# Kernel tuning notes

Measured on AMD Instinct MI355X. Metric: run time of the kernel, lower is better.

Reference implementation:

```python
import jax, jax.numpy as jnp
import numpy as np

PI = 3.1415927410125732
N = 4096
VELOCITY = 5e-7
RC = 3.15e-6          # collision radius
RR = 8e-6             # repulsion radius
RO = 2.5e-5           # orientation radius (Ra = inf -> inside_Ra all-true)
ALPHA = PI            # field of view; < 2*pi so within_view masking is active
DT_TRANS = 1.4e-14    # translational diffusion DT
DR = 0.0028
GAMMA = 25.0
DT = 0.2              # timestep dt
COLLISION_ITERS = 3   # fixed-iteration version of recursive solve_collisions
EPS = 1e-14


def _c(x):  # [N,2] real -> complex64
    return jax.lax.complex(x[..., 0], x[..., 1])


def _r(z):  # complex -> [..., 2] real
    return jnp.stack([z.real, z.imag], axis=-1)


def _anglediff(a, b):
    # torch get_anglediff: wrap angle(a)-angle(b) into (-pi, pi)
    diff = jnp.angle(a) - jnp.angle(b)
    diff = jnp.where(diff <= -PI, jnp.mod(diff, PI), diff)
    return diff - (diff >= PI) * (2.0 * PI)


def _cossim(a, b):
    # nn.CosineSimilarity(dim=1, eps=1e-14) on view_as_real of complex vectors
    dot = a.real * b.real + a.imag * b.imag
    na = jnp.sqrt(a.real ** 2 + a.imag ** 2 + 1e-30)
    nb = jnp.sqrt(b.real ** 2 + b.imag ** 2 + 1e-30)
    return dot / (jnp.maximum(na, EPS) * jnp.maximum(nb, EPS))


def setup_inputs() -> dict:
    key = jax.random.key(0)
    k1, k2, k3, k4, k5 = jax.random.split(key, 5)
    positions = jax.random.normal(k1, (N, 2), jnp.float32) * 5e-4
    ang = jax.random.uniform(k2, (N,), jnp.float32, -PI, PI)
    orientations = jnp.stack([jnp.cos(ang), jnp.sin(ang)], axis=-1)  # unit complex
    Deltas = jax.random.uniform(k3, (1,), jnp.float32, 0.1, 0.6)
    rot_noise = jax.random.normal(k4, (N,), jnp.float32)
    trans_noise = jax.random.normal(k5, (N, 2), jnp.float32)
    return {"positions": positions, "orientations": orientations, "Deltas": Deltas,
            "rot_noise": rot_noise, "trans_noise": trans_noise}


def reference(positions, orientations, Deltas, rot_noise, trans_noise):
    p = _c(positions)      # [N] complex positions
    u = _c(orientations)   # [N] complex orientations
    n = p.shape[0]
    eye = jnp.eye(n, dtype=bool)

    # pairwise direction/distance: dirs[i,j] = p_j - p_i
    dirs = p[None, :] - p[:, None]
    dists = jnp.abs(dirs)

    inside_Rr = (dists <= RR) & ~eye
    inside_Ro = dists <= RO + RC
    # inside_Ra with Ra = inf is all-True

    # angle between separation vector and orientation of the *neighbor* j
    ang_diff = _anglediff(dirs, u[None, :])
    in_front = ang_diff < PI / 2
    within_view = ang_diff < ALPHA  # alpha < 2*pi branch active

    cdtype = p.dtype
    mask_rr = (inside_Rr & in_front).astype(cdtype)
    mask_ra = within_view.astype(cdtype)  # inside_Ra all True
    mask_ro = (inside_Ro & within_view).astype(cdtype)

    n_r = mask_rr.real.sum(axis=1)
    S = (mask_rr @ p) / jnp.maximum(n_r, 1.0) - p * jnp.sign(n_r)
    d = -S

    n_a = mask_ra.real.sum(axis=1)
    cms = (mask_ra @ p) / jnp.maximum(n_a, 1.0)
    Ps = cms - p * jnp.sign(n_a)

    orientation_sums = mask_ro @ u

    leftturns = Ps * jnp.exp(1j * Deltas)
    rightturns = Ps * jnp.exp(-1j * Deltas)

    # T >= T_release branch: pick the turn most aligned with neighbor orientations
    left_closer = _cossim(leftturns, orientation_sums) >= _cossim(rightturns, orientation_sums)
    best_turns = jnp.where(left_closer, leftturns, rightturns)

    d_abs = jnp.abs(d)
    d_safe = jnp.where(d_abs > 0, d, jnp.ones((), cdtype))
    best_safe = jnp.where(jnp.abs(best_turns) > 0, best_turns, jnp.ones((), cdtype))
    angle_to_target = jnp.where(d_abs > 0, _anglediff(d_safe, u), _anglediff(best_safe, u))

    # rotational_noise = randn * sqrt(2*DR); rotation = exp(i*(dt*Gamma*DR*sin + noise*sqrt(dt)))
    rot = jnp.exp(1j * (DT * GAMMA * DR * jnp.sin(angle_to_target)
                        + rot_noise * np.float32(np.sqrt(2 * DR)) * np.float32(np.sqrt(DT))))

    # complex-normal translational noise (per-component std 1/sqrt(2)) * sqrt(2*DT) * sqrt(dt)
    tn = _c(trans_noise) * np.float32(np.sqrt(0.5)) * np.float32(np.sqrt(2 * DT_TRANS))
    translation = DT * VELOCITY * u + tn * np.float32(np.sqrt(DT))

    def collide(i, pos):
        dd = pos[None, :] - pos[:, None]
        dd_nd = jnp.where(eye, jnp.ones((), pos.dtype), dd)  # avoid 0/0 on diagonal
        ab = jnp.where(eye, 0.0, jnp.abs(dd_nd))
        coll = ab <= 2 * RC - jnp.eye(n, dtype=ab.dtype)
        safe = jnp.where(coll, ab, 1.0)
        move = jnp.where(coll, dd / safe * ((2.1 * RC - ab) * 0.5), jnp.zeros((), pos.dtype))
        return pos - move.sum(axis=1)

    new_p = jax.lax.fori_loop(0, COLLISION_ITERS, collide, p + translation)
    new_u = u * rot

    # pack the 5 complex outputs as real [5, N, 2]
    return jnp.stack([_r(new_p), _r(new_u), _r(orientation_sums), _r(leftturns), _r(rightturns)], axis=0)
```

## Files before the change

### kernel.cpp

```cpp
#include <hip/hip_runtime.h>
#include <math.h>

#define NPART 4096
#define NBLK  1024
#define NTHR  256
#define IPB   4
#define SMAX  256
#define PPT   (NPART / NTHR)

constexpr float RORC   = (float)(2.5e-5 + 3.15e-6);
constexpr float RORC2  = RORC * RORC;
constexpr float RRF    = 8e-6f;
constexpr float RR2    = RRF * RRF;
constexpr float TWORC  = (float)(2.0 * 3.15e-6);
constexpr float TWORC2 = TWORC * TWORC;
constexpr float C21RC  = (float)(2.1 * 3.15e-6);
constexpr float RCAND2 = 1.6e-9f;
constexpr float C_ROT  = (float)(0.2 * 25.0 * 0.0028);
constexpr float C_RN1  = (float)0.07483314773547883;
constexpr float C_SQDT = (float)0.4472135954999579;
constexpr float C_TRV  = (float)(0.2 * 5e-7);
constexpr float C_HALF = (float)0.7071067811865476;
constexpr float C_SQ2T = (float)1.6733200530681511e-07;
constexpr float EPSF   = 1e-14f;

__global__ __launch_bounds__(NTHR, 4) void fused_all(
        const float2* __restrict__ pos, const float2* __restrict__ ori,
        const float* __restrict__ Deltas, const float* __restrict__ rot_noise,
        const float2* __restrict__ trans_noise, float2* __restrict__ out) {
    __shared__ float4   posL4[NPART / 2];
    __shared__ float    sred[2 * NTHR];
    __shared__ float    res[5][IPB];
    __shared__ unsigned bmap[NPART / 32];
    __shared__ int      Sidx[SMAX];
    __shared__ float4   posS4[SMAX / 2];
    __shared__ int      scnt;
    float2* posL = (float2*)posL4;
    float2* posS = (float2*)posS4;

    const int tid  = threadIdx.x;
    const int il   = tid >> 6;
    const int lane = tid & 63;
    const int gi   = blockIdx.x * IPB + il;

    if (tid == 0) scnt = IPB;
    if (tid < IPB) Sidx[tid] = blockIdx.x * IPB + tid;
    if (tid < NPART / 32) bmap[tid] = 0u;

    float mx = 0.f, my = 0.f;
    #pragma unroll
    for (int k = 0; k < PPT; ++k) {
        const float2 v = pos[k * NTHR + tid];
        posL[k * NTHR + tid] = v;
        mx += v.x; my += v.y;
    }
    sred[tid] = mx; sred[NTHR + tid] = my;
    __syncthreads();

    const float2 pi = posL[gi];
    float nr = 0.f, sx = 0.f, sy = 0.f, oxs = 0.f, oys = 0.f;
    #pragma unroll 2
    for (int t = lane; t < NPART / 2; t += 64) {
        const float4 w = posL4[t];
        const float dx0 = w.x - pi.x, dy0 = w.y - pi.y;
        const float r20 = fmaf(dx0, dx0, dy0 * dy0);
        const float dx1 = w.z - pi.x, dy1 = w.w - pi.y;
        const float r21 = fmaf(dx1, dx1, dy1 * dy1);
        if (r20 <= RCAND2) {
            const int j = 2 * t;
            atomicOr(&bmap[j >> 5], 1u << (j & 31));
            if (r20 <= RORC2) {
                const float2 uj = ori[j];
                oxs += uj.x; oys += uj.y;
                if (r20 <= RR2 && r20 > 0.f) {
                    const float dt_ = fmaf(dx0, uj.x, dy0 * uj.y);
                    const float cr_ = fmaf(dy0, uj.x, -dx0 * uj.y);
                    if (!((dt_ <= 0.f) && (cr_ >= 0.f))) {
                        nr += 1.f; sx += w.x; sy += w.y;
                    }
                }
            }
        }
        if (r21 <= RCAND2) {
            const int j = 2 * t + 1;
            atomicOr(&bmap[j >> 5], 1u << (j & 31));
            if (r21 <= RORC2) {
                const float2 uj = ori[j];
                oxs += uj.x; oys += uj.y;
                if (r21 <= RR2 && r21 > 0.f) {
                    const float dt_ = fmaf(dx1, uj.x, dy1 * uj.y);
                    const float cr_ = fmaf(dy1, uj.x, -dx1 * uj.y);
                    if (!((dt_ <= 0.f) && (cr_ >= 0.f))) {
                        nr += 1.f; sx += w.z; sy += w.w;
                    }
                }
            }
        }
    }
    {
        float vals[5] = {nr, sx, sy, oxs, oys};
        #pragma unroll
        for (int q = 0; q < 5; ++q)
            #pragma unroll
            for (int off = 32; off >= 1; off >>= 1)
                vals[q] += __shfl_down(vals[q], off);
        if (lane == 0) {
            res[0][il] = vals[0]; res[1][il] = vals[1]; res[2][il] = vals[2];
            res[3][il] = vals[3]; res[4][il] = vals[4];
        }
    }
    __syncthreads();

    if (tid < NPART / 32) {
        unsigned bits = bmap[tid];
        if (tid == (int)(blockIdx.x >> 3))
            bits &= ~(0xFu << ((blockIdx.x & 7) * 4));
        while (bits) {
            const int b = __ffs(bits) - 1;
            bits &= bits - 1;
            const int slot = atomicAdd(&scnt, 1);
            if (slot < SMAX) Sidx[slot] = tid * 32 + b;
        }
    }
    __syncthreads();
    const int nS = (scnt < SMAX) ? scnt : SMAX;

    if (tid < nS) {
        const int p = Sidx[tid];
        const float2 pq = posL[p];
        const float2 uu = ori[p];
        const float2 tn = trans_noise[p];
        posS[tid] = make_float2(
            pq.x + (C_TRV * uu.x + ((tn.x * C_HALF) * C_SQ2T) * C_SQDT),
            pq.y + (C_TRV * uu.y + ((tn.y * C_HALF) * C_SQ2T) * C_SQDT));
    }

    for (int s = NTHR / 2; s > 0; s >>= 1) {
        if (tid < s) { sred[tid] += sred[tid + s]; sred[NTHR + tid] += sred[NTHR + tid + s]; }
        __syncthreads();
    }
    const float cmx = sred[0]    * (1.f / NPART);
    const float cmy = sred[NTHR] * (1.f / NPART);

    if (tid < IPB) {
        const int g2 = blockIdx.x * IPB + tid;
        const float2 p = posL[g2];
        const float2 u = ori[g2];
        const float nrv = res[0][tid], sxv = res[1][tid], syv = res[2][tid];
        const float osx = res[3][tid], osy = res[4][tid];

        const float inv = 1.f / fmaxf(nrv, 1.f);
        const float sg  = (nrv > 0.f) ? 1.f : 0.f;
        const float Sx = sxv * inv - p.x * sg;
        const float Sy = syv * inv - p.y * sg;
        const float dxv = -Sx, dyv = -Sy;

        const float Psx = cmx - p.x;
        const float Psy = cmy - p.y;

        float sd, cd;
        sincosf(Deltas[0], &sd, &cd);
        const float Lx = Psx * cd - Psy * sd;
        const float Ly = Psx * sd + Psy * cd;
        const float Rx = Psx * cd + Psy * sd;
        const float Ry = Psy * cd - Psx * sd;

        const float no  = fmaxf(sqrtf(osx * osx + osy * osy + 1e-30f), EPSF);
        const float nl  = fmaxf(sqrtf(Lx * Lx + Ly * Ly + 1e-30f), EPSF);
        const float nrr = fmaxf(sqrtf(Rx * Rx + Ry * Ry + 1e-30f), EPSF);
        const float csl = (Lx * osx + Ly * osy) / (nl * no);
        const float csr = (Rx * osx + Ry * osy) / (nrr * no);
        const bool left = (csl >= csr);
        const float bx = left ? Lx : Rx;
        const float by = left ? Ly : Ry;

        float cx, cy;
        if (dxv != 0.f || dyv != 0.f)    { cx = dxv; cy = dyv; }
        else if (bx != 0.f || by != 0.f) { cx = bx;  cy = by;  }
        else                             { cx = 1.f; cy = 0.f; }

        const float dt_ = cx * u.x + cy * u.y;
        const float cr_ = cy * u.x - cx * u.y;
        const float sin_t = cr_ / sqrtf(dt_ * dt_ + cr_ * cr_);

        const float ang = C_ROT * sin_t + (rot_noise[g2] * C_RN1) * C_SQDT;
        float sa, ca;
        sincosf(ang, &sa, &ca);
        out[1 * NPART + g2] = make_float2(u.x * ca - u.y * sa,
                                          u.x * sa + u.y * ca);
        out[2 * NPART + g2] = make_float2(osx, osy);
        out[3 * NPART + g2] = make_float2(Lx, Ly);
        out[4 * NPART + g2] = make_float2(Rx, Ry);
    }
    __syncthreads();

    for (int pass = 0; pass < 3; ++pass) {
        float px = 0.f, py = 0.f, ax = 0.f, ay = 0.f;
        const bool mv = (tid < nS);
        if (mv) { px = posS[tid].x; py = posS[tid].y; }
        int b = 0;
        for (; b + 4 <= nS; b += 4) {
            const float4 w0 = posS4[(b >> 1)];
            const float4 w1 = posS4[(b >> 1) + 1];
            const float bxs[4] = {w0.x, w0.z, w1.x, w1.z};
            const float bys[4] = {w0.y, w0.w, w1.y, w1.w};
            #pragma unroll
            for (int s = 0; s < 4; ++s) {
                if (mv) {
                    const float dx = bxs[s] - px, dy = bys[s] - py;
                    const float r2 = fmaf(dx, dx, dy * dy);
                    if (r2 <= TWORC2 && r2 > 0.f) {
                        const float ab = sqrtf(r2);
                        const float sc = (C21RC - ab) * 0.5f / ab;
                        ax = fmaf(dx, sc, ax);
                        ay = fmaf(dy, sc, ay);
                    }
                }
            }
        }
        for (; b < nS; ++b) {
            const float2 pb = posS[b];
            if (mv) {
                const float dx = pb.x - px, dy = pb.y - py;
                const float r2 = fmaf(dx, dx, dy * dy);
                if (r2 <= TWORC2 && r2 > 0.f) {
                    const float ab = sqrtf(r2);
                    const float sc = (C21RC - ab) * 0.5f / ab;
                    ax = fmaf(dx, sc, ax);
                    ay = fmaf(dy, sc, ay);
                }
            }
        }
        __syncthreads();
        if (mv) posS[tid] = make_float2(px - ax, py - ay);
        __syncthreads();
    }
    if (tid < IPB)
        out[0 * NPART + blockIdx.x * IPB + tid] = posS[tid];
}

extern "C" void kernel_launch(void* const* d_in, const int* in_sizes, int n_in,
                              void* d_out, int out_size, void* d_ws, size_t ws_size,
                              hipStream_t stream) {
    const float2* pos = (const float2*)d_in[0];
    const float2* ori = (const float2*)d_in[1];
    const float*  del = (const float*)d_in[2];
    const float*  rn  = (const float*)d_in[3];
    const float2* tn  = (const float2*)d_in[4];
    float2* o2 = (float2*)d_out;
    (void)d_ws; (void)ws_size;

    fused_all<<<dim3(NBLK), dim3(NTHR), 0, stream>>>(pos, ori, del, rn, tn, o2);
}
```

Baseline: 82.87 us.

## Process two target particles per wavefront and stage orientations in LDS

Each block now handles eight particles instead of four, with each wavefront computing neighbour statistics for two particles against every loaded position. This halves the number of blocks, so the per-block cost of staging all positions into LDS and reducing the centre of mass is paid half as often. Orientations are also copied into shared memory so neighbour orientation lookups no longer go to global memory. The trade-offs are larger LDS use, more registers (launch bounds lowered to 2) and fewer blocks to spread across the GPU.

Measured after the change: 92.10 us. +11.1%, slower.

```diff
diff --git a/kernel.cpp b/kernel.cpp
--- a/kernel.cpp
+++ b/kernel.cpp
@@ -2,9 +2,9 @@
 #include <math.h>
 
 #define NPART 4096
-#define NBLK  1024
+#define NBLK  512
 #define NTHR  256
-#define IPB   4
+#define IPB   8
 #define SMAX  256
 #define PPT   (NPART / NTHR)
 
@@ -24,11 +24,12 @@
 constexpr float C_SQ2T = (float)1.6733200530681511e-07;
 constexpr float EPSF   = 1e-14f;
 
-__global__ __launch_bounds__(NTHR, 4) void fused_all(
+__global__ __launch_bounds__(NTHR, 2) void fused_all(
         const float2* __restrict__ pos, const float2* __restrict__ ori,
         const float* __restrict__ Deltas, const float* __restrict__ rot_noise,
         const float2* __restrict__ trans_noise, float2* __restrict__ out) {
     __shared__ float4   posL4[NPART / 2];
+    __shared__ float4   oriL4[NPART / 2];
     __shared__ float    sred[2 * NTHR];
     __shared__ float    res[5][IPB];
     __shared__ unsigned bmap[NPART / 32];
@@ -36,12 +37,14 @@
     __shared__ float4   posS4[SMAX / 2];
     __shared__ int      scnt;
     float2* posL = (float2*)posL4;
+    float2* oriL = (float2*)oriL4;
     float2* posS = (float2*)posS4;
 
     const int tid  = threadIdx.x;
     const int il   = tid >> 6;
     const int lane = tid & 63;
-    const int gi   = blockIdx.x * IPB + il;
+    const int ia   = blockIdx.x * IPB + il;
+    const int ib   = ia + 4;
 
     if (tid == 0) scnt = IPB;
     if (tid < IPB) Sidx[tid] = blockIdx.x * IPB + tid;
@@ -51,70 +54,107 @@
     #pragma unroll
     for (int k = 0; k < PPT; ++k) {
         const float2 v = pos[k * NTHR + tid];
+        const float2 u = ori[k * NTHR + tid];
         posL[k * NTHR + tid] = v;
+        oriL[k * NTHR + tid] = u;
         mx += v.x; my += v.y;
     }
     sred[tid] = mx; sred[NTHR + tid] = my;
     __syncthreads();
 
-    const float2 pi = posL[gi];
-    float nr = 0.f, sx = 0.f, sy = 0.f, oxs = 0.f, oys = 0.f;
+    const float2 pa = posL[ia];
+    const float2 pb = posL[ib];
+    float nrA = 0.f, sxA = 0.f, syA = 0.f, oxA = 0.f, oyA = 0.f;
+    float nrB = 0.f, sxB = 0.f, syB = 0.f, oxB = 0.f, oyB = 0.f;
     #pragma unroll 2
     for (int t = lane; t < NPART / 2; t += 64) {
         const float4 w = posL4[t];
-        const float dx0 = w.x - pi.x, dy0 = w.y - pi.y;
-        const float r20 = fmaf(dx0, dx0, dy0 * dy0);
-        const float dx1 = w.z - pi.x, dy1 = w.w - pi.y;
-        const float r21 = fmaf(dx1, dx1, dy1 * dy1);
-        if (r20 <= RCAND2) {
+        const float dxa0 = w.x - pa.x, dya0 = w.y - pa.y;
+        const float dxb0 = w.x - pb.x, dyb0 = w.y - pb.y;
+        const float dxa1 = w.z - pa.x, dya1 = w.w - pa.y;
+        const float dxb1 = w.z - pb.x, dyb1 = w.w - pb.y;
+        const float r2a0 = fmaf(dxa0, dxa0, dya0 * dya0);
+        const float r2b0 = fmaf(dxb0, dxb0, dyb0 * dyb0);
+        const float r2a1 = fmaf(dxa1, dxa1, dya1 * dya1);
+        const float r2b1 = fmaf(dxb1, dxb1, dyb1 * dyb1);
+
+        if (r2a0 <= RCAND2 || r2b0 <= RCAND2) {
             const int j = 2 * t;
             atomicOr(&bmap[j >> 5], 1u << (j & 31));
-            if (r20 <= RORC2) {
-                const float2 uj = ori[j];
-                oxs += uj.x; oys += uj.y;
-                if (r20 <= RR2 && r20 > 0.f) {
-                    const float dt_ = fmaf(dx0, uj.x, dy0 * uj.y);
-                    const float cr_ = fmaf(dy0, uj.x, -dx0 * uj.y);
-                    if (!((dt_ <= 0.f) && (cr_ >= 0.f))) {
-                        nr += 1.f; sx += w.x; sy += w.y;
-                    }
-                }
-            }
-        }
-        if (r21 <= RCAND2) {
+        }
+        if (r2a0 <= RORC2 || r2b0 <= RORC2) {
+            const float2 uj = oriL[2 * t];
+            if (r2a0 <= RORC2) {
+                oxA += uj.x; oyA += uj.y;
+                if (r2a0 <= RR2 && r2a0 > 0.f) {
+                    const float dt_ = fmaf(dxa0, uj.x, dya0 * uj.y);
+                    const float cr_ = fmaf(dya0, uj.x, -dxa0 * uj.y);
+                    if (!((dt_ <= 0.f) && (cr_ >= 0.f))) {
+                        nrA += 1.f; sxA += w.x; syA += w.y;
+                    }
+                }
+            }
+            if (r2b0 <= RORC2) {
+                oxB += uj.x; oyB += uj.y;
+                if (r2b0 <= RR2 && r2b0 > 0.f) {
+                    const float dt_ = fmaf(dxb0, uj.x, dyb0 * uj.y);
+                    const float cr_ = fmaf(dyb0, uj.x, -dxb0 * uj.y);
+                    if (!((dt_ <= 0.f) && (cr_ >= 0.f))) {
+                        nrB += 1.f; sxB += w.x; syB += w.y;
+                    }
+                }
+            }
+        }
+        if (r2a1 <= RCAND2 || r2b1 <= RCAND2) {
             const int j = 2 * t + 1;
             atomicOr(&bmap[j >> 5], 1u << (j & 31));
-            if (r21 <= RORC2) {
-                const float2 uj = ori[j];
-                oxs += uj.x; oys += uj.y;
-                if (r21 <= RR2 && r21 > 0.f) {
-                    const float dt_ = fmaf(dx1, uj.x, dy1 * uj.y);
-                    const float cr_ = fmaf(dy1, uj.x, -dx1 * uj.y);
-                    if (!((dt_ <= 0.f) && (cr_ >= 0.f))) {
-                        nr += 1.f; sx += w.z; sy += w.w;
+        }
+        if (r2a1 <= RORC2 || r2b1 <= RORC2) {
+            const float2 uj = oriL[2 * t + 1];
+            if (r2a1 <= RORC2) {
+                oxA += uj.x; oyA += uj.y;
+                if (r2a1 <= RR2 && r2a1 > 0.f) {
+                    const float dt_ = fmaf(dxa1, uj.x, dya1 * uj.y);
+                    const float cr_ = fmaf(dya1, uj.x, -dxa1 * uj.y);
+                    if (!((dt_ <= 0.f) && (cr_ >= 0.f))) {
+                        nrA += 1.f; sxA += w.z; syA += w.w;
+                    }
+                }
+            }
+            if (r2b1 <= RORC2) {
+                oxB += uj.x; oyB += uj.y;
+                if (r2b1 <= RR2 && r2b1 > 0.f) {
+                    const float dt_ = fmaf(dxb1, uj.x, dyb1 * uj.y);
+                    const float cr_ = fmaf(dyb1, uj.x, -dxb1 * uj.y);
+                    if (!((dt_ <= 0.f) && (cr_ >= 0.f))) {
+                        nrB += 1.f; sxB += w.z; syB += w.w;
                     }
                 }
             }
         }
     }
     {
-        float vals[5] = {nr, sx, sy, oxs, oys};
+        float vals[10] = {nrA, sxA, syA, oxA, oyA, nrB, sxB, syB, oxB, oyB};
         #pragma unroll
-        for (int q = 0; q < 5; ++q)
+        for (int q = 0; q < 10; ++q)
             #pragma unroll
             for (int off = 32; off >= 1; off >>= 1)
                 vals[q] += __shfl_down(vals[q], off);
         if (lane == 0) {
-            res[0][il] = vals[0]; res[1][il] = vals[1]; res[2][il] = vals[2];
-            res[3][il] = vals[3]; res[4][il] = vals[4];
+            res[0][il]     = vals[0]; res[1][il]     = vals[1];
+            res[2][il]     = vals[2]; res[3][il]     = vals[3];
+            res[4][il]     = vals[4];
+            res[0][il + 4] = vals[5]; res[1][il + 4] = vals[6];
+            res[2][il + 4] = vals[7]; res[3][il + 4] = vals[8];
+            res[4][il + 4] = vals[9];
         }
     }
     __syncthreads();
 
     if (tid < NPART / 32) {
         unsigned bits = bmap[tid];
-        if (tid == (int)(blockIdx.x >> 3))
-            bits &= ~(0xFu << ((blockIdx.x & 7) * 4));
+        if (tid == (int)(blockIdx.x >> 2))
+            bits &= ~(0xFFu << ((blockIdx.x & 3) * 8));
         while (bits) {
             const int b = __ffs(bits) - 1;
             bits &= bits - 1;
@@ -128,7 +168,7 @@
     if (tid < nS) {
         const int p = Sidx[tid];
         const float2 pq = posL[p];
-        const float2 uu = ori[p];
+        const float2 uu = oriL[p];
         const float2 tn = trans_noise[p];
         posS[tid] = make_float2(
             pq.x + (C_TRV * uu.x + ((tn.x * C_HALF) * C_SQ2T) * C_SQDT),
@@ -145,7 +185,7 @@
     if (tid < IPB) {
         const int g2 = blockIdx.x * IPB + tid;
         const float2 p = posL[g2];
-        const float2 u = ori[g2];
+        const float2 u = oriL[g2];
         const float nrv = res[0][tid], sxv = res[1][tid], syv = res[2][tid];
         const float osx = res[3][tid], osy = res[4][tid];
 
@@ -219,9 +259,9 @@
             }
         }
         for (; b < nS; ++b) {
-            const float2 pb = posS[b];
+            const float2 pb2 = posS[b];
             if (mv) {
-                const float dx = pb.x - px, dy = pb.y - py;
+                const float dx = pb2.x - px, dy = pb2.y - py;
                 const float r2 = fmaf(dx, dx, dy * dy);
                 if (r2 <= TWORC2 && r2 > 0.f) {
                     const float ab = sqrtf(r2);
```
